# Kernel tuning notes

Hardware: AMD Instinct MI355X
Metric: run time of the kernel (lower is better)

## Reference

```python
import jax, jax.numpy as jnp
import numpy as np

C = 128          # hidden width hard-coded in DirModelToFace
EPS = 1e-5       # BatchNorm1d eps


def sparse_bmm(rows, cols, vals, x, num_rows):
    """Batched sparse @ dense: COO (rows, cols, vals) shared across batch.
    x: [B, K, c] -> [B, num_rows, c]."""
    def one(xb):
        return jax.ops.segment_sum(xb[cols] * vals[:, None], rows, num_segments=num_rows)
    return jax.vmap(one)(x)


def conv1x1_prebn(x, gamma, beta, W, b):
    # GraphConv1x1(batch_norm='pre'): BN (training stats over B*N rows) then Linear
    mean = x.mean((0, 1))
    var = x.var((0, 1))  # biased, as torch BN uses for normalization
    xh = (x - mean) * jax.lax.rsqrt(var + EPS) * gamma + beta
    return xh @ W + b


def dir_block(Di, DiA, v, f, g, be, W, b):
    # DirResNet2 (res_f=False): quaternionic Dirac message passing
    B, N, _ = v.shape
    Fn = f.shape[1]
    msg_v = sparse_bmm(*DiA, f.reshape(B, 4 * Fn, C // 4), 4 * N).reshape(B, N, C)
    x = jax.nn.elu(jnp.concatenate([v, msg_v], axis=-1))
    v_out = v + conv1x1_prebn(x, g[0], be[0], W[0], b[0])
    msg_f = sparse_bmm(*Di, v_out.reshape(B, 4 * N, C // 4), 4 * Fn).reshape(B, Fn, C)
    x = jax.nn.elu(jnp.concatenate([f, msg_f], axis=-1))
    f_out = conv1x1_prebn(x, g[1], be[1], W[1], b[1])  # no residual on f
    return v_out, f_out


def avg_block(mask, v, g, be, W, b):
    # AvgResNet2: masked global average message
    x = v
    for j in range(2):
        x = jax.nn.elu(x)
        x_avg = (mask * x).sum(1, keepdims=True) / mask.sum(1, keepdims=True)
        x = jnp.concatenate([x, jnp.broadcast_to(x_avg, x.shape)], axis=-1)
        x = conv1x1_prebn(x, g[j], be[j], W[j], b[j])
    return x + v


def setup_inputs() -> dict:
    key = jax.random.key(0)
    ks = jax.random.split(key, 10)
    B, N, Fn = 4, 12000, 24000
    nnz = 48 * Fn  # 3 vertices per face x 4x4 quaternion block
    inputs = jax.random.normal(ks[0], (B, N, 3), jnp.float32)
    mask = jnp.ones((B, N, 1), jnp.float32)
    Di_rows = jax.random.randint(ks[1], (nnz,), 0, 4 * Fn, jnp.int32)
    Di_cols = jax.random.randint(ks[2], (nnz,), 0, 4 * N, jnp.int32)
    Di_vals = jax.random.normal(ks[3], (nnz,), jnp.float32) * 0.1
    DiA_rows = jax.random.randint(ks[4], (nnz,), 0, 4 * N, jnp.int32)
    DiA_cols = jax.random.randint(ks[5], (nnz,), 0, 4 * Fn, jnp.int32)
    DiA_vals = jax.random.normal(ks[6], (nnz,), jnp.float32) * 0.1
    W1 = jax.random.normal(ks[7], (3, C), jnp.float32) / np.sqrt(3.0)
    b1 = jnp.zeros((C,), jnp.float32)
    rn_gamma = jnp.ones((16, 2, 2 * C), jnp.float32)
    rn_beta = jnp.zeros((16, 2, 2 * C), jnp.float32)
    rn_W = jax.random.normal(ks[8], (16, 2, 2 * C, C), jnp.float32) / np.sqrt(2.0 * C)
    rn_b = jnp.zeros((16, 2, C), jnp.float32)
    g2 = jnp.ones((C,), jnp.float32)
    be2 = jnp.zeros((C,), jnp.float32)
    W2 = jax.random.normal(ks[9], (C, 1), jnp.float32) / np.sqrt(1.0 * C)
    b2 = jnp.zeros((1,), jnp.float32)
    return dict(inputs=inputs, mask=mask,
                Di_rows=Di_rows, Di_cols=Di_cols, Di_vals=Di_vals,
                DiA_rows=DiA_rows, DiA_cols=DiA_cols, DiA_vals=DiA_vals,
                W1=W1, b1=b1, rn_gamma=rn_gamma, rn_beta=rn_beta, rn_W=rn_W, rn_b=rn_b,
                g2=g2, be2=be2, W2=W2, b2=b2, num_faces=24000)


def reference(inputs, mask, Di_rows, Di_cols, Di_vals, DiA_rows, DiA_cols, DiA_vals,
              W1, b1, rn_gamma, rn_beta, rn_W, rn_b, g2, be2, W2, b2, num_faces):
    B, N, _ = inputs.shape
    v = inputs @ W1 + b1                       # conv1 (batch_norm=None)
    f = jnp.zeros((B, num_faces, C), v.dtype)  # face features start at zero
    Di = (Di_rows, Di_cols, Di_vals)
    DiA = (DiA_rows, DiA_cols, DiA_vals)
    for i in range(16):
        if i % 2 == 0:
            v, f = dir_block(Di, DiA, v, f, rn_gamma[i], rn_beta[i], rn_W[i], rn_b[i])
        else:
            v = avg_block(mask, v, rn_gamma[i], rn_beta[i], rn_W[i], rn_b[i])
    x = jax.nn.elu(f)
    return conv1x1_prebn(x, g2, be2, W2, b2)   # conv2 (batch_norm='pre')
```

## Files before the change

### kernel.cpp

```cpp
#include <hip/hip_runtime.h>
#include <hip/hip_fp16.h>
#include <math.h>


#define EPS 1e-5f

typedef float floatx4 __attribute__((ext_vector_type(4)));
typedef short shortx8 __attribute__((ext_vector_type(8)));

__device__ __forceinline__ float eluf(float x) { return x > 0.f ? x : expm1f(x); }
__device__ __forceinline__ float4 elu4(float4 v) {
    v.x = eluf(v.x); v.y = eluf(v.y); v.z = eluf(v.z); v.w = eluf(v.w); return v;
}
__device__ __forceinline__ short f2bf(float x) {
    unsigned u = __builtin_bit_cast(unsigned, x);
    u = u + 0x7FFFu + ((u >> 16) & 1u);
    return (short)(u >> 16);
}
__device__ __forceinline__ float bf2f(short h) {
    unsigned u = ((unsigned)(unsigned short)h) << 16;
    return __builtin_bit_cast(float, u);
}
__device__ __forceinline__ void split2(float x, short& hi, short& lo) {
    unsigned u = __builtin_bit_cast(unsigned, x);
    hi = (short)(u >> 16);
    float r = x - bf2f(hi);
    lo = (short)(__builtin_bit_cast(unsigned, r) >> 16);
}

__global__ void conv1_kernel(const float* __restrict__ in, const float* __restrict__ W1,
                             const float* __restrict__ b1, float* __restrict__ v,
                             __half* __restrict__ vH, int N, float* __restrict__ Sout,
                             const float* __restrict__ mask, float* __restrict__ msum,
                             int nConv) {
    __shared__ float sh[4];
    int t = threadIdx.x;
    if (blockIdx.x >= nConv) {
        int b = blockIdx.x - nConv;
        float s = 0.f;
        for (int n = t; n < N; n += 256) s += mask[(size_t)b * N + n];
        for (int o = 32; o > 0; o >>= 1) s += __shfl_down(s, o);
        if ((t & 63) == 0) sh[t >> 6] = s;
        __syncthreads();
        if (t == 0) msum[b] = sh[0] + sh[1] + sh[2] + sh[3];
        return;
    }
    int c = t & 127, half = t >> 7;
    int r0 = blockIdx.x * 64;
    float w0 = W1[c], w1 = W1[128 + c], w2 = W1[256 + c], bb = b1[c];
    float s1 = 0.f, s2 = 0.f;
    for (int k = 0; k < 32; ++k) {
        int r = r0 + half + 2 * k;
        float x0 = in[r * 3 + 0], x1 = in[r * 3 + 1], x2 = in[r * 3 + 2];
        float val = bb + x0 * w0 + x1 * w1 + x2 * w2;
        v[(size_t)r * 128 + c] = val;
        int b = r / N, vert = r - b * N;
        vH[(size_t)(4 * vert + (c >> 5)) * 128 + b * 32 + (c & 31)] = __float2half(val);
        float e = eluf(val);
        s1 += e; s2 += e * e;
    }
    atomicAdd(&Sout[c], s1);
    atomicAdd(&Sout[256 + c], s2);
}


__global__ void hist2_kernel(const int* __restrict__ rowsA, const int* __restrict__ rowsD,
                             int* __restrict__ cntA, int* __restrict__ cntD) {
    int e = blockIdx.x * 256 + threadIdx.x;
    if (blockIdx.y == 0) atomicAdd(&cntA[rowsA[e]], 1);
    else atomicAdd(&cntD[rowsD[e]], 1);
}

__global__ void partial2_kernel(const int* __restrict__ cntA, const int* __restrict__ cntD,
                                int* __restrict__ partA, int* __restrict__ partD,
                                int RA, int RD) {
    const int* counts = blockIdx.y ? cntD : cntA;
    int* partials = blockIdx.y ? partD : partA;
    int R = blockIdx.y ? RD : RA;
    int t = threadIdx.x;
    int base = blockIdx.x * 1024 + t * 4;
    int s = 0;
#pragma unroll
    for (int j = 0; j < 4; ++j) { int i = base + j; if (i < R) s += counts[i]; }
    __shared__ int sh[256];
    sh[t] = s; __syncthreads();
    for (int st = 128; st > 0; st >>= 1) {
        if (t < st) sh[t] += sh[t + st];
        __syncthreads();
    }
    if (t == 0) partials[blockIdx.x] = sh[0];
}

__global__ void scanp2_kernel(int* __restrict__ partA, int* __restrict__ partD,
                              int* __restrict__ ptrA, int* __restrict__ ptrD,
                              int PA, int PD, int RA, int RD, int total) {
    int* partials = blockIdx.y ? partD : partA;
    int* rowptr = blockIdx.y ? ptrD : ptrA;
    int P = blockIdx.y ? PD : PA;
    int R = blockIdx.y ? RD : RA;
    __shared__ int sh[256];
    int t = threadIdx.x;
    int v = (t < P) ? partials[t] : 0;
    sh[t] = v; __syncthreads();
    for (int st = 1; st < 256; st <<= 1) {
        int tmp = (t >= st) ? sh[t - st] : 0;
        __syncthreads();
        sh[t] += tmp;
        __syncthreads();
    }
    if (t < P) partials[t] = sh[t] - v;
    if (t == 0) rowptr[R] = total;
}

__global__ void apply2_kernel(int* __restrict__ cntA, int* __restrict__ cntD,
                              const int* __restrict__ partA, const int* __restrict__ partD,
                              int* __restrict__ ptrA, int* __restrict__ ptrD,
                              int RA, int RD) {
    int* counts = blockIdx.y ? cntD : cntA;
    const int* partials = blockIdx.y ? partD : partA;
    int* rowptr = blockIdx.y ? ptrD : ptrA;
    int R = blockIdx.y ? RD : RA;
    int t = threadIdx.x;
    int base = blockIdx.x * 1024 + t * 4;
    int c[4]; int s = 0;
#pragma unroll
    for (int j = 0; j < 4; ++j) { int i = base + j; c[j] = (i < R) ? counts[i] : 0; s += c[j]; }
    __shared__ int sh[256];
    sh[t] = s; __syncthreads();
    for (int st = 1; st < 256; st <<= 1) {
        int tmp = (t >= st) ? sh[t - st] : 0;
        __syncthreads();
        sh[t] += tmp;
        __syncthreads();
    }
    int off = partials[blockIdx.x] + sh[t] - s;
#pragma unroll
    for (int j = 0; j < 4; ++j) {
        int i = base + j;
        if (i < R) { rowptr[i] = off; counts[i] = off; }
        off += c[j];
    }
}

__global__ void scatter2_kernel(const int* __restrict__ rowsA, const int* __restrict__ colsA,
                                const float* __restrict__ valsA,
                                const int* __restrict__ rowsD, const int* __restrict__ colsD,
                                const float* __restrict__ valsD,
                                int* __restrict__ fillA, int* __restrict__ fillD,
                                int2* __restrict__ edgesA, int2* __restrict__ edgesD) {
    int e = blockIdx.x * 256 + threadIdx.x;
    if (blockIdx.y == 0) {
        int p = atomicAdd(&fillA[rowsA[e]], 1);
        edgesA[p] = make_int2(colsA[e], __float_as_int(valsA[e]));
    } else {
        int p = atomicAdd(&fillD[rowsD[e]], 1);
        edgesD[p] = make_int2(colsD[e], __float_as_int(valsD[e]));
    }
}

template <int DIR>
__global__ __launch_bounds__(1024) void spmm_csr_kernel(
    const int* __restrict__ rowptr, const int2* __restrict__ edges,
    const __half2* __restrict__ xH, float* __restrict__ y, int R4,
    float* __restrict__ Sout) {
    int t = threadIdx.x;
    int waveId = blockIdx.x * 16 + (t >> 6);
    int lane = t & 63;
    int b = lane >> 4, cp = lane & 15;
    const __half2* xb = xH + b * 16 + cp;
    size_t rs = (size_t)R4 * 32;
    __shared__ float red[256];
    if (t < 256) red[t] = 0.f;
    __syncthreads();
#pragma unroll
    for (int rr = 0; rr < 2; ++rr) {
        int r = waveId * 2 + rr;
        int e0 = rowptr[r], e1 = rowptr[r + 1];
        float ax = 0.f, ay = 0.f;
        int e = e0;
        for (; e + 4 <= e1; e += 4) {
            int2 E0 = edges[e], E1 = edges[e + 1], E2 = edges[e + 2], E3 = edges[e + 3];
            __half2 g0 = xb[(size_t)E0.x * 64];
            __half2 g1 = xb[(size_t)E1.x * 64];
            __half2 g2 = xb[(size_t)E2.x * 64];
            __half2 g3 = xb[(size_t)E3.x * 64];
            float v0 = __int_as_float(E0.y), v1 = __int_as_float(E1.y);
            float v2 = __int_as_float(E2.y), v3 = __int_as_float(E3.y);
            float2 f0 = __half22float2(g0), f1 = __half22float2(g1);
            float2 f2 = __half22float2(g2), f3 = __half22float2(g3);
            ax += v0 * f0.x; ay += v0 * f0.y;
            ax += v1 * f1.x; ay += v1 * f1.y;
            ax += v2 * f2.x; ay += v2 * f2.y;
            ax += v3 * f3.x; ay += v3 * f3.y;
        }
        for (; e < e1; ++e) {
            int2 E = edges[e];
            __half2 g = xb[(size_t)E.x * 64];
            float v = __int_as_float(E.y);
            float2 f = __half22float2(g);
            ax += v * f.x; ay += v * f.y;
        }
        *(float2*)&y[(size_t)b * rs + (size_t)r * 32 + cp * 2] = make_float2(ax, ay);
        float ea = eluf(ax), eb = eluf(ay);
        float s1a = ea, s2a = ea * ea, s1b = eb, s2b = eb * eb;
        s1a += __shfl_xor(s1a, 16); s1a += __shfl_xor(s1a, 32);
        s2a += __shfl_xor(s2a, 16); s2a += __shfl_xor(s2a, 32);
        s1b += __shfl_xor(s1b, 16); s1b += __shfl_xor(s1b, 32);
        s2b += __shfl_xor(s2b, 16); s2b += __shfl_xor(s2b, 32);
        if (lane < 16) {
            int ch = (r & 3) * 32 + cp * 2;
            atomicAdd(&red[ch], s1a);
            atomicAdd(&red[ch + 1], s1b);
            atomicAdd(&red[128 + ch], s2a);
            atomicAdd(&red[128 + ch + 1], s2b);
        }
    }
    __syncthreads();
    if (t < 128) atomicAdd(&Sout[128 + t], red[t]);
    else if (t < 256) atomicAdd(&Sout[384 + (t - 128)], red[t]);
}

template <int MODEB>
__global__ __launch_bounds__(256) void gemm_mfma(
    const float* __restrict__ A, const float* __restrict__ Bs,
    const float* __restrict__ S, const float* __restrict__ gvec,
    const float* __restrict__ bevec, const float* __restrict__ Wfull,
    const float* __restrict__ bvec, const float* __restrict__ resid,
    float* __restrict__ out, __half* __restrict__ shadow,
    float* __restrict__ Sout, const float* __restrict__ mask,
    float* __restrict__ avgout, const float* __restrict__ avgacc,
    const float* __restrict__ msum, float invR, int rowsPerBatch) {
    __shared__ short Bsh[128 * 40];
    __shared__ short Bsl[128 * 40];
    __shared__ float sS[256];
    __shared__ float sMS[256];
    __shared__ float avgLDS[512];
    __shared__ float bparr[256];
    __shared__ float bparrX[2][256];
    __shared__ float bpF2[2][128];
    const int t = threadIdx.x;
    const int lane = t & 63;
    const int wave = t >> 6;
    const int rowBase = blockIdx.x * 128 + wave * 32;
    const int m = lane & 15;
    const int kq = lane >> 4;
    constexpr int kbEnd = (MODEB == 0) ? 8 : 4;
    const int colW = t & 127;
    const int qs0 = t >> 7;
    const int bBlk = (blockIdx.x * 128) / rowsPerBatch;

    {
        int k = t;
        float mean, var;
        if (MODEB == 1 && k >= 128) {
            int c = k - 128;
            float a0 = avgacc[c] / msum[0];
            float a1 = avgacc[128 + c] / msum[1];
            float a2 = avgacc[256 + c] / msum[2];
            float a3 = avgacc[384 + c] / msum[3];
            avgLDS[c] = a0; avgLDS[128 + c] = a1;
            avgLDS[256 + c] = a2; avgLDS[384 + c] = a3;
            mean = 0.25f * (a0 + a1 + a2 + a3);
            var = 0.25f * (a0 * a0 + a1 * a1 + a2 * a2 + a3 * a3) - mean * mean;
        } else {
            mean = S[k] * invR;
            var = S[256 + k] * invR - mean * mean;
        }
        float s = gvec[k] / sqrtf(var + EPS);
        sS[k] = s;
        sMS[k] = bevec[k] - mean * s;
    }

    floatx4 acc[2][8];
#pragma unroll
    for (int i = 0; i < 2; ++i)
#pragma unroll
        for (int j = 0; j < 8; ++j) acc[i][j] = {0.f, 0.f, 0.f, 0.f};

    float bpp = 0.f;
    for (int kb = 0; kb < kbEnd; ++kb) {
        const int k0 = kb * 32 + kq * 8;
        __syncthreads();
#pragma unroll
        for (int i = 0; i < 2; ++i) {
            const int qs = qs0 + 2 * i;
            shortx8 hv, lv;
#pragma unroll
            for (int j = 0; j < 8; ++j) {
                int k = kb * 32 + qs * 8 + j;
                float w = Wfull[(size_t)k * 128 + colW];
                float wp = sS[k] * w;
                short h = f2bf(wp);
                hv[j] = h;
                lv[j] = f2bf(wp - bf2f(h));
                bpp += sMS[k] * w;
            }
            *(shortx8*)&Bsh[colW * 40 + qs * 8] = hv;
            *(shortx8*)&Bsl[colW * 40 + qs * 8] = lv;
        }
        shortx8 ah[2], al[2];
#pragma unroll
        for (int rg = 0; rg < 2; ++rg) {
            int row = rowBase + rg * 16 + m;
            float4 p, q;
            if (kb < 4) {
                p = elu4(*(const float4*)&A[(size_t)row * 128 + k0]);
                q = elu4(*(const float4*)&A[(size_t)row * 128 + k0 + 4]);
            } else {
                int kk = k0 - 128;
                p = elu4(*(const float4*)&Bs[(size_t)row * 128 + kk]);
                q = elu4(*(const float4*)&Bs[(size_t)row * 128 + kk + 4]);
            }
            float x[8] = {p.x, p.y, p.z, p.w, q.x, q.y, q.z, q.w};
#pragma unroll
            for (int j = 0; j < 8; ++j) { short h, l; split2(x[j], h, l); ah[rg][j] = h; al[rg][j] = l; }
        }
        __syncthreads();
#pragma unroll
        for (int ct = 0; ct < 8; ++ct) {
            const int co = (ct * 16 + m) * 40 + kq * 8;
            shortx8 bh = *(const shortx8*)&Bsh[co];
            shortx8 bl = *(const shortx8*)&Bsl[co];
#pragma unroll
            for (int rg = 0; rg < 2; ++rg) {
                acc[rg][ct] = __builtin_amdgcn_mfma_f32_16x16x32_bf16(ah[rg], bh, acc[rg][ct], 0, 0, 0);
                acc[rg][ct] = __builtin_amdgcn_mfma_f32_16x16x32_bf16(ah[rg], bl, acc[rg][ct], 0, 0, 0);
                acc[rg][ct] = __builtin_amdgcn_mfma_f32_16x16x32_bf16(al[rg], bh, acc[rg][ct], 0, 0, 0);
            }
        }
    }

    float bps0 = 0.f, bps1 = 0.f;
    if (MODEB == 2) {
        for (int j = 0; j < 64; ++j) {
            int k = 128 + qs0 * 64 + j;
            bps0 += sMS[k] * Wfull[(size_t)k * 128 + colW];
        }
        bps1 = bps0;
    } else if (MODEB == 1) {
        const int b0 = bBlk, b1 = (bBlk + 1 < 4) ? bBlk + 1 : 3;
        for (int j = 0; j < 64; ++j) {
            int k = 128 + qs0 * 64 + j;
            float w = Wfull[(size_t)k * 128 + colW];
            float sw = sS[k] * w;
            float base = sMS[k] * w;
            bps0 += base + avgLDS[b0 * 128 + (k - 128)] * sw;
            bps1 += base + avgLDS[b1 * 128 + (k - 128)] * sw;
        }
    }
    bparr[t] = bpp;
    bparrX[0][t] = bps0;
    bparrX[1][t] = bps1;
    __syncthreads();
    if (t < 128) {
        float common = bvec[t] + bparr[t] + bparr[t + 128];
        bpF2[0][t] = common + bparrX[0][t] + bparrX[0][t + 128];
        bpF2[1][t] = common + bparrX[1][t] + bparrX[1][t + 128];
    }
    __syncthreads();

    float mk8[8]; int ib8[8];
#pragma unroll
    for (int rg = 0; rg < 2; ++rg)
#pragma unroll
        for (int r = 0; r < 4; ++r) {
            int row = rowBase + rg * 16 + kq * 4 + r;
            ib8[rg * 4 + r] = (row >= (bBlk + 1) * rowsPerBatch) ? 1 : 0;
            if (avgout) mk8[rg * 4 + r] = mask[row];
        }
    float cs1[8], cs2[8], av0[8], av1[8];
#pragma unroll
    for (int ct = 0; ct < 8; ++ct) { cs1[ct] = 0.f; cs2[ct] = 0.f; av0[ct] = 0.f; av1[ct] = 0.f; }
#pragma unroll
    for (int ct = 0; ct < 8; ++ct) {
        int col = ct * 16 + m;
        float bb0 = bpF2[0][col], bb1 = bpF2[1][col];
#pragma unroll
        for (int rg = 0; rg < 2; ++rg) {
#pragma unroll
            for (int r = 0; r < 4; ++r) {
                int row = rowBase + rg * 16 + kq * 4 + r;
                size_t o = (size_t)row * 128 + col;
                float v = acc[rg][ct][r] + (ib8[rg * 4 + r] ? bb1 : bb0);
                if (resid) v += resid[o];
                out[o] = v;
                if (shadow) {
                    int b = row / rowsPerBatch, vert = row - b * rowsPerBatch;
                    shadow[(size_t)(4 * vert + (col >> 5)) * 128 + b * 32 + (col & 31)] =
                        __float2half(v);
                }
                float e = eluf(v);
                cs1[ct] += e; cs2[ct] += e * e;
                if (avgout) {
                    float me = mk8[rg * 4 + r] * e;
                    if (ib8[rg * 4 + r]) av1[ct] += me; else av0[ct] += me;
                }
            }
        }
    }
    if (Sout) {
        __syncthreads();
        float* red = (float*)Bsh;
        float* redv = (float*)Bsl;
        red[t] = 0.f;
        if (avgout) redv[t] = 0.f;
        __syncthreads();
#pragma unroll
        for (int ct = 0; ct < 8; ++ct) {
            cs1[ct] += __shfl_xor(cs1[ct], 16); cs1[ct] += __shfl_xor(cs1[ct], 32);
            cs2[ct] += __shfl_xor(cs2[ct], 16); cs2[ct] += __shfl_xor(cs2[ct], 32);
            if (avgout) {
                av0[ct] += __shfl_xor(av0[ct], 16); av0[ct] += __shfl_xor(av0[ct], 32);
                av1[ct] += __shfl_xor(av1[ct], 16); av1[ct] += __shfl_xor(av1[ct], 32);
            }
        }
        if (kq == 0) {
#pragma unroll
            for (int ct = 0; ct < 8; ++ct) {
                atomicAdd(&red[ct * 16 + m], cs1[ct]);
                atomicAdd(&red[128 + ct * 16 + m], cs2[ct]);
                if (avgout) {
                    atomicAdd(&redv[ct * 16 + m], av0[ct]);
                    atomicAdd(&redv[128 + ct * 16 + m], av1[ct]);
                }
            }
        }
        __syncthreads();
        if (t < 128) atomicAdd(&Sout[t], red[t]);
        else atomicAdd(&Sout[256 + (t - 128)], red[t]);
        if (avgout) {
            int plane = t >> 7, col = t & 127;
            int b = bBlk + plane;
            if (b < 4) atomicAdd(&avgout[b * 128 + col], redv[t]);
        }
    }
}

__global__ void fold_final(const float* __restrict__ S, const float* __restrict__ g2,
                           const float* __restrict__ be2, const float* __restrict__ W2,
                           const float* __restrict__ b2, float* __restrict__ W2p, float invR) {
    __shared__ float red[128];
    int c = threadIdx.x;
    float mean = S[c] * invR;
    float var = S[256 + c] * invR - mean * mean;
    float s = g2[c] / sqrtf(var + EPS);
    float w = W2[c];
    W2p[c] = s * w;
    red[c] = (be2[c] - mean * s) * w;
    __syncthreads();
    for (int st = 64; st > 0; st >>= 1) {
        if (c < st) red[c] += red[c + st];
        __syncthreads();
    }
    if (c == 0) W2p[128] = b2[0] + red[0];
}

__global__ void final_out_kernel(const float* __restrict__ f, const float* __restrict__ W2p,
                                 float* __restrict__ out) {
    int t = threadIdx.x;
    int w = t >> 6, lane = t & 63;
    float wa = W2p[lane], wb = W2p[64 + lane], bb = W2p[128];
    int base = blockIdx.x * 16 + w * 4;
#pragma unroll
    for (int rr = 0; rr < 4; ++rr) {
        int row = base + rr;
        float a = eluf(f[(size_t)row * 128 + lane]) * wa +
                  eluf(f[(size_t)row * 128 + 64 + lane]) * wb;
        for (int off = 32; off > 0; off >>= 1) a += __shfl_down(a, off);
        if (lane == 0) out[row] = a + bb;
    }
}

extern "C" void kernel_launch(void* const* d_in, const int* in_sizes, int n_in,
                              void* d_out, int out_size, void* d_ws, size_t ws_size,
                              hipStream_t stream) {
    const float* inputs = (const float*)d_in[0];
    const float* mask = (const float*)d_in[1];
    const int* Di_rows = (const int*)d_in[2];
    const int* Di_cols = (const int*)d_in[3];
    const float* Di_vals = (const float*)d_in[4];
    const int* DiA_rows = (const int*)d_in[5];
    const int* DiA_cols = (const int*)d_in[6];
    const float* DiA_vals = (const float*)d_in[7];
    const float* W1 = (const float*)d_in[8];
    const float* b1 = (const float*)d_in[9];
    const float* rn_gamma = (const float*)d_in[10];
    const float* rn_beta = (const float*)d_in[11];
    const float* rn_W = (const float*)d_in[12];
    const float* rn_b = (const float*)d_in[13];
    const float* g2 = (const float*)d_in[14];
    const float* be2 = (const float*)d_in[15];
    const float* W2 = (const float*)d_in[16];
    const float* b2 = (const float*)d_in[17];
    float* out = (float*)d_out;

    const int B = 4;
    const int BN = in_sizes[1];
    const int N = BN / B;
    const int BF = out_size;
    const int Fn = BF / B;
    const int nnz = in_sizes[2];
    const int RA = 4 * N;
    const int RD = 4 * Fn;

    float* ws = (float*)d_ws;
    size_t off = 0;
    float* vA = ws + off;  off += (size_t)BN * 128;
    float* fA = ws + off;  off += (size_t)BF * 128;
    float* msg = ws + off; off += (size_t)BF * 128;
    __half* vH = (__half*)(ws + off); off += (size_t)RA * 128 / 2;
    __half* fH = (__half*)(ws + off); off += (size_t)RD * 128 / 2;
    int* ptrA    = (int*)(ws + off);  off += (size_t)RA + 4;
    int2* edgesA = (int2*)(ws + off); off += (size_t)nnz * 2;
    int* ptrD    = (int*)(ws + off);  off += (size_t)RD + 4;
    int2* edgesD = (int2*)(ws + off); off += (size_t)nnz * 2;
    int* cntA    = (int*)(ws + off);  off += (size_t)RA;
    int* cntD    = (int*)(ws + off);  off += (size_t)RD;
    int* partA   = (int*)(ws + off);  off += 256;
    int* partD   = (int*)(ws + off);  off += 256;
    float* Sarena = ws + off; off += 33 * 512;
    float* Aarena = ws + off; off += 16 * 512;
    float* msum = ws + off;   off += 4;
    float* W2p = ws + off; off += 132;

    const int eBlocks = nnz / 256;
    const int PA = (RA + 1023) / 1024;
    const int PD = (RD + 1023) / 1024;

    hipMemsetAsync(Sarena, 0, (33 * 512 + 16 * 512) * 4, stream);
    hipMemsetAsync(fA, 0, (size_t)BF * 128 * 4, stream);
    hipMemsetAsync(cntA, 0, (size_t)(RA + RD) * 4, stream);

    hist2_kernel<<<dim3(eBlocks, 2), 256, 0, stream>>>(DiA_rows, Di_rows, cntA, cntD);
    partial2_kernel<<<dim3(PD, 2), 256, 0, stream>>>(cntA, cntD, partA, partD, RA, RD);
    scanp2_kernel<<<dim3(1, 2), 256, 0, stream>>>(partA, partD, ptrA, ptrD, PA, PD,
                                                  RA, RD, nnz);
    apply2_kernel<<<dim3(PD, 2), 256, 0, stream>>>(cntA, cntD, partA, partD, ptrA, ptrD,
                                                   RA, RD);
    scatter2_kernel<<<dim3(eBlocks, 2), 256, 0, stream>>>(DiA_rows, DiA_cols, DiA_vals,
                                                          Di_rows, Di_cols, Di_vals,
                                                          cntA, cntD, edgesA, edgesD);

    auto slot = [&](int i, int j) { return Sarena + 512 * (2 * i + j); };
    float* Sfinal = Sarena + 512 * 32;

    conv1_kernel<<<BN / 64 + B, 256, 0, stream>>>(inputs, W1, b1, vA, vH, N, slot(0, 0),
                                                  mask, msum, BN / 64);

    for (int i = 0; i < 15; ++i) {
        if ((i & 1) == 0) {
            const float* g0 = rn_gamma + (size_t)(i * 2 + 0) * 256;
            const float* be0 = rn_beta + (size_t)(i * 2 + 0) * 256;
            const float* Wl0 = rn_W + (size_t)(i * 2 + 0) * 256 * 128;
            const float* bl0 = rn_b + (size_t)(i * 2 + 0) * 128;
            const float* g1 = rn_gamma + (size_t)(i * 2 + 1) * 256;
            const float* be1 = rn_beta + (size_t)(i * 2 + 1) * 256;
            const float* Wl1 = rn_W + (size_t)(i * 2 + 1) * 256 * 128;
            const float* bl1 = rn_b + (size_t)(i * 2 + 1) * 128;
            float* SoutV = (i < 14) ? slot(i + 1, 0) : nullptr;
            float* avgV = (i < 14) ? (Aarena + 512 * i) : nullptr;

            if (i == 0) {
                gemm_mfma<2><<<BN / 128, 256, 0, stream>>>(vA, nullptr, slot(0, 0), g0, be0,
                                                           Wl0, bl0, vA, vA, vH, SoutV, mask,
                                                           avgV, nullptr, nullptr, 1.f / BN,
                                                           N);
            } else {
                spmm_csr_kernel<0><<<RA / 32, 1024, 0, stream>>>(ptrA, edgesA,
                                                                 (const __half2*)fH, msg,
                                                                 RA, slot(i, 0));
                gemm_mfma<0><<<BN / 128, 256, 0, stream>>>(vA, msg, slot(i, 0), g0, be0,
                                                           Wl0, bl0, vA, vA, vH, SoutV, mask,
                                                           avgV, nullptr, nullptr, 1.f / BN,
                                                           N);
            }

            spmm_csr_kernel<1><<<RD / 32, 1024, 0, stream>>>(ptrD, edgesD,
                                                             (const __half2*)vH, msg, RD,
                                                             slot(i, 1));
            gemm_mfma<0><<<BF / 128, 256, 0, stream>>>(fA, msg, slot(i, 1), g1, be1, Wl1,
                                                       bl1, nullptr, fA, fH,
                                                       (i < 14) ? slot(i + 2, 1) : Sfinal,
                                                       nullptr, nullptr, nullptr, nullptr,
                                                       1.f / BF, Fn);
        } else {
            for (int j = 0; j < 2; ++j) {
                const float* g = rn_gamma + (size_t)(i * 2 + j) * 256;
                const float* be = rn_beta + (size_t)(i * 2 + j) * 256;
                const float* Wlw = rn_W + (size_t)(i * 2 + j) * 256 * 128;
                const float* bl = rn_b + (size_t)(i * 2 + j) * 128;
                const float* src = (j == 0) ? vA : msg;
                float* dst = (j == 0) ? msg : vA;
                const float* resid = (j == 0) ? nullptr : vA;
                __half* shadow = (j == 0) ? nullptr : vH;
                float* SoutP = (j == 0) ? slot(i, 1) : slot(i + 1, 0);
                float* avgO = (j == 0) ? (Aarena + 512 * i) : nullptr;
                const float* avgacc = Aarena + 512 * (i - 1 + j);

                gemm_mfma<1><<<BN / 128, 256, 0, stream>>>(src, nullptr, slot(i, j), g, be,
                                                           Wlw, bl, resid, dst, shadow,
                                                           SoutP, mask, avgO, avgacc, msum,
                                                           1.f / BN, N);
            }
        }
    }

    fold_final<<<1, 128, 0, stream>>>(Sfinal, g2, be2, W2, b2, W2p, 1.f / BF);
    final_out_kernel<<<BF / 16, 256, 0, stream>>>(fA, W2p, out);
}
```

Measured before the change: 4.151 ms.

## Prefold weights into MFMA fragment layout once; apply BN to activations instead

A new prefold kernel converts every layer's weight matrix to split hi/lo bf16 in MFMA fragment order once per call. The GEMM then loads B fragments straight from global memory, removing the per-block LDS staging, syncs and weight folding. BatchNorm scale and shift move onto the activations, and the avg-block broadcast term becomes real K columns instead of a bias correction. The cost is that MODEB 1 and 2 now always run 8 k-blocks, the i==0 case multiplies against zeros, and occupancy is raised to 2 blocks per SIMD via launch bounds.

```diff
diff --git a/kernel.cpp b/kernel.cpp
--- a/kernel.cpp
+++ b/kernel.cpp
@@ -26,6 +26,28 @@
     hi = (short)(u >> 16);
     float r = x - bf2f(hi);
     lo = (short)(__builtin_bit_cast(unsigned, r) >> 16);
+}
+
+__global__ void prefold_kernel(const float* __restrict__ rnW, short* __restrict__ Wh,
+                               short* __restrict__ Wl) {
+    int L = blockIdx.y;
+    int id = blockIdx.x * 256 + threadIdx.x;
+    int chunk = id >> 6, lane = id & 63;
+    int kb = chunk >> 3, ct = chunk & 7, kq = lane >> 4, m = lane & 15;
+    const float* W = rnW + (size_t)L * 32768;
+    shortx8 hv, lv;
+#pragma unroll
+    for (int j = 0; j < 8; ++j) {
+        int k = kb * 32 + kq * 8 + j;
+        int c = ct * 16 + m;
+        float w = W[k * 128 + c];
+        short h = f2bf(w);
+        hv[j] = h;
+        lv[j] = f2bf(w - bf2f(h));
+    }
+    size_t o = (size_t)L * 32768 + (size_t)id * 8;
+    *(shortx8*)&Wh[o] = hv;
+    *(shortx8*)&Wl[o] = lv;
 }
 
 __global__ void conv1_kernel(const float* __restrict__ in, const float* __restrict__ W1,
@@ -221,32 +243,27 @@
 }
 
 template <int MODEB>
-__global__ __launch_bounds__(256) void gemm_mfma(
+__global__ __launch_bounds__(256, 2) void gemm_mfma(
     const float* __restrict__ A, const float* __restrict__ Bs,
     const float* __restrict__ S, const float* __restrict__ gvec,
-    const float* __restrict__ bevec, const float* __restrict__ Wfull,
-    const float* __restrict__ bvec, const float* __restrict__ resid,
-    float* __restrict__ out, __half* __restrict__ shadow,
-    float* __restrict__ Sout, const float* __restrict__ mask,
-    float* __restrict__ avgout, const float* __restrict__ avgacc,
-    const float* __restrict__ msum, float invR, int rowsPerBatch) {
-    __shared__ short Bsh[128 * 40];
-    __shared__ short Bsl[128 * 40];
+    const float* __restrict__ bevec, const short* __restrict__ Wh,
+    const short* __restrict__ Wl, const float* __restrict__ bvec,
+    const float* __restrict__ resid, float* __restrict__ out,
+    __half* __restrict__ shadow, float* __restrict__ Sout,
+    const float* __restrict__ mask, float* __restrict__ avgout,
+    const float* __restrict__ avgacc, const float* __restrict__ msum,
+    float invR, int rowsPerBatch) {
     __shared__ float sS[256];
     __shared__ float sMS[256];
     __shared__ float avgLDS[512];
-    __shared__ float bparr[256];
-    __shared__ float bparrX[2][256];
-    __shared__ float bpF2[2][128];
+    __shared__ float red[256];
+    __shared__ float redv[256];
     const int t = threadIdx.x;
     const int lane = t & 63;
     const int wave = t >> 6;
     const int rowBase = blockIdx.x * 128 + wave * 32;
     const int m = lane & 15;
     const int kq = lane >> 4;
-    constexpr int kbEnd = (MODEB == 0) ? 8 : 4;
-    const int colW = t & 127;
-    const int qs0 = t >> 7;
     const int bBlk = (blockIdx.x * 128) / rowsPerBatch;
 
     {
@@ -270,6 +287,7 @@
         sS[k] = s;
         sMS[k] = bevec[k] - mean * s;
     }
+    __syncthreads();
 
     floatx4 acc[2][8];
 #pragma unroll
@@ -277,50 +295,51 @@
 #pragma unroll
         for (int j = 0; j < 8; ++j) acc[i][j] = {0.f, 0.f, 0.f, 0.f};
 
-    float bpp = 0.f;
-    for (int kb = 0; kb < kbEnd; ++kb) {
+#pragma unroll 2
+    for (int kb = 0; kb < 8; ++kb) {
         const int k0 = kb * 32 + kq * 8;
-        __syncthreads();
-#pragma unroll
-        for (int i = 0; i < 2; ++i) {
-            const int qs = qs0 + 2 * i;
-            shortx8 hv, lv;
+        shortx8 ah[2], al[2];
+#pragma unroll
+        for (int rg = 0; rg < 2; ++rg) {
+            const int row = rowBase + rg * 16 + m;
+            float x[8];
+            if (kb < 4) {
+                float4 p = elu4(*(const float4*)&A[(size_t)row * 128 + k0]);
+                float4 q = elu4(*(const float4*)&A[(size_t)row * 128 + k0 + 4]);
+                x[0] = p.x; x[1] = p.y; x[2] = p.z; x[3] = p.w;
+                x[4] = q.x; x[5] = q.y; x[6] = q.z; x[7] = q.w;
+            } else if (MODEB == 0) {
+                const int kk = k0 - 128;
+                float4 p = elu4(*(const float4*)&Bs[(size_t)row * 128 + kk]);
+                float4 q = elu4(*(const float4*)&Bs[(size_t)row * 128 + kk + 4]);
+                x[0] = p.x; x[1] = p.y; x[2] = p.z; x[3] = p.w;
+                x[4] = q.x; x[5] = q.y; x[6] = q.z; x[7] = q.w;
+            } else if (MODEB == 1) {
+                const int kk = k0 - 128;
+                const int b = row / rowsPerBatch;
+                float4 p = *(const float4*)&avgLDS[b * 128 + kk];
+                float4 q = *(const float4*)&avgLDS[b * 128 + kk + 4];
+                x[0] = p.x; x[1] = p.y; x[2] = p.z; x[3] = p.w;
+                x[4] = q.x; x[5] = q.y; x[6] = q.z; x[7] = q.w;
+            } else {
+#pragma unroll
+                for (int j = 0; j < 8; ++j) x[j] = 0.f;
+            }
 #pragma unroll
             for (int j = 0; j < 8; ++j) {
-                int k = kb * 32 + qs * 8 + j;
-                float w = Wfull[(size_t)k * 128 + colW];
-                float wp = sS[k] * w;
-                short h = f2bf(wp);
-                hv[j] = h;
-                lv[j] = f2bf(wp - bf2f(h));
-                bpp += sMS[k] * w;
-            }
-            *(shortx8*)&Bsh[colW * 40 + qs * 8] = hv;
-            *(shortx8*)&Bsl[colW * 40 + qs * 8] = lv;
-        }
-        shortx8 ah[2], al[2];
-#pragma unroll
-        for (int rg = 0; rg < 2; ++rg) {
-            int row = rowBase + rg * 16 + m;
-            float4 p, q;
-            if (kb < 4) {
-                p = elu4(*(const float4*)&A[(size_t)row * 128 + k0]);
-                q = elu4(*(const float4*)&A[(size_t)row * 128 + k0 + 4]);
-            } else {
-                int kk = k0 - 128;
-                p = elu4(*(const float4*)&Bs[(size_t)row * 128 + kk]);
-                q = elu4(*(const float4*)&Bs[(size_t)row * 128 + kk + 4]);
-            }
-            float x[8] = {p.x, p.y, p.z, p.w, q.x, q.y, q.z, q.w};
-#pragma unroll
-            for (int j = 0; j < 8; ++j) { short h, l; split2(x[j], h, l); ah[rg][j] = h; al[rg][j] = l; }
-        }
-        __syncthreads();
+                const int k = k0 + j;
+                float ap = sS[k] * x[j] + sMS[k];
+                short h, l;
+                split2(ap, h, l);
+                ah[rg][j] = h;
+                al[rg][j] = l;
+            }
+        }
 #pragma unroll
         for (int ct = 0; ct < 8; ++ct) {
-            const int co = (ct * 16 + m) * 40 + kq * 8;
-            shortx8 bh = *(const shortx8*)&Bsh[co];
-            shortx8 bl = *(const shortx8*)&Bsl[co];
+            const size_t wo = ((size_t)(kb * 8 + ct) * 64 + lane) * 8;
+            shortx8 bh = *(const shortx8*)&Wh[wo];
+            shortx8 bl = *(const shortx8*)&Wl[wo];
 #pragma unroll
             for (int rg = 0; rg < 2; ++rg) {
                 acc[rg][ct] = __builtin_amdgcn_mfma_f32_16x16x32_bf16(ah[rg], bh, acc[rg][ct], 0, 0, 0);
@@ -330,58 +349,31 @@
         }
     }
 
-    float bps0 = 0.f, bps1 = 0.f;
-    if (MODEB == 2) {
-        for (int j = 0; j < 64; ++j) {
-            int k = 128 + qs0 * 64 + j;
-            bps0 += sMS[k] * Wfull[(size_t)k * 128 + colW];
-        }
-        bps1 = bps0;
-    } else if (MODEB == 1) {
-        const int b0 = bBlk, b1 = (bBlk + 1 < 4) ? bBlk + 1 : 3;
-        for (int j = 0; j < 64; ++j) {
-            int k = 128 + qs0 * 64 + j;
-            float w = Wfull[(size_t)k * 128 + colW];
-            float sw = sS[k] * w;
-            float base = sMS[k] * w;
-            bps0 += base + avgLDS[b0 * 128 + (k - 128)] * sw;
-            bps1 += base + avgLDS[b1 * 128 + (k - 128)] * sw;
-        }
-    }
-    bparr[t] = bpp;
-    bparrX[0][t] = bps0;
-    bparrX[1][t] = bps1;
-    __syncthreads();
-    if (t < 128) {
-        float common = bvec[t] + bparr[t] + bparr[t + 128];
-        bpF2[0][t] = common + bparrX[0][t] + bparrX[0][t + 128];
-        bpF2[1][t] = common + bparrX[1][t] + bparrX[1][t + 128];
-    }
-    __syncthreads();
-
     float mk8[8]; int ib8[8];
-#pragma unroll
-    for (int rg = 0; rg < 2; ++rg)
-#pragma unroll
-        for (int r = 0; r < 4; ++r) {
-            int row = rowBase + rg * 16 + kq * 4 + r;
-            ib8[rg * 4 + r] = (row >= (bBlk + 1) * rowsPerBatch) ? 1 : 0;
-            if (avgout) mk8[rg * 4 + r] = mask[row];
-        }
+    if (avgout) {
+#pragma unroll
+        for (int rg = 0; rg < 2; ++rg)
+#pragma unroll
+            for (int r = 0; r < 4; ++r) {
+                int row = rowBase + rg * 16 + kq * 4 + r;
+                mk8[rg * 4 + r] = mask[row];
+                ib8[rg * 4 + r] = (row >= (bBlk + 1) * rowsPerBatch) ? 1 : 0;
+            }
+    }
     float cs1[8], cs2[8], av0[8], av1[8];
 #pragma unroll
     for (int ct = 0; ct < 8; ++ct) { cs1[ct] = 0.f; cs2[ct] = 0.f; av0[ct] = 0.f; av1[ct] = 0.f; }
 #pragma unroll
     for (int ct = 0; ct < 8; ++ct) {
         int col = ct * 16 + m;
-        float bb0 = bpF2[0][col], bb1 = bpF2[1][col];
+        float bb = bvec[col];
 #pragma unroll
         for (int rg = 0; rg < 2; ++rg) {
 #pragma unroll
             for (int r = 0; r < 4; ++r) {
                 int row = rowBase + rg * 16 + kq * 4 + r;
                 size_t o = (size_t)row * 128 + col;
-                float v = acc[rg][ct][r] + (ib8[rg * 4 + r] ? bb1 : bb0);
+                float v = acc[rg][ct][r] + bb;
                 if (resid) v += resid[o];
                 out[o] = v;
                 if (shadow) {
@@ -400,8 +392,6 @@
     }
     if (Sout) {
         __syncthreads();
-        float* red = (float*)Bsh;
-        float* redv = (float*)Bsl;
         red[t] = 0.f;
         if (avgout) redv[t] = 0.f;
         __syncthreads();
@@ -522,6 +512,8 @@
     float* Aarena = ws + off; off += 16 * 512;
     float* msum = ws + off;   off += 4;
     float* W2p = ws + off; off += 132;
+    short* Wh = (short*)(ws + off); off += (size_t)32 * 32768 / 2;
+    short* Wl = (short*)(ws + off); off += (size_t)32 * 32768 / 2;
 
     const int eBlocks = nnz / 256;
     const int PA = (RA + 1023) / 1024;
@@ -530,6 +522,8 @@
     hipMemsetAsync(Sarena, 0, (33 * 512 + 16 * 512) * 4, stream);
     hipMemsetAsync(fA, 0, (size_t)BF * 128 * 4, stream);
     hipMemsetAsync(cntA, 0, (size_t)(RA + RD) * 4, stream);
+
+    prefold_kernel<<<dim3(16, 32), 256, 0, stream>>>(rn_W, Wh, Wl);
 
     hist2_kernel<<<dim3(eBlocks, 2), 256, 0, stream>>>(DiA_rows, Di_rows, cntA, cntD);
     partial2_kernel<<<dim3(PD, 2), 256, 0, stream>>>(cntA, cntD, partA, partD, RA, RD);
@@ -547,39 +541,41 @@
     conv1_kernel<<<BN / 64 + B, 256, 0, stream>>>(inputs, W1, b1, vA, vH, N, slot(0, 0),
                                                   mask, msum, BN / 64);
 
+    auto WhL = [&](int i, int j) { return Wh + (size_t)(i * 2 + j) * 32768; };
+    auto WlL = [&](int i, int j) { return Wl + (size_t)(i * 2 + j) * 32768; };
+
     for (int i = 0; i < 15; ++i) {
         if ((i & 1) == 0) {
             const float* g0 = rn_gamma + (size_t)(i * 2 + 0) * 256;
             const float* be0 = rn_beta + (size_t)(i * 2 + 0) * 256;
-            const float* Wl0 = rn_W + (size_t)(i * 2 + 0) * 256 * 128;
             const float* bl0 = rn_b + (size_t)(i * 2 + 0) * 128;
             const float* g1 = rn_gamma + (size_t)(i * 2 + 1) * 256;
             const float* be1 = rn_beta + (size_t)(i * 2 + 1) * 256;
-            const float* Wl1 = rn_W + (size_t)(i * 2 + 1) * 256 * 128;
             const float* bl1 = rn_b + (size_t)(i * 2 + 1) * 128;
             float* SoutV = (i < 14) ? slot(i + 1, 0) : nullptr;
             float* avgV = (i < 14) ? (Aarena + 512 * i) : nullptr;
 
             if (i == 0) {
                 gemm_mfma<2><<<BN / 128, 256, 0, stream>>>(vA, nullptr, slot(0, 0), g0, be0,
-                                                           Wl0, bl0, vA, vA, vH, SoutV, mask,
-                                                           avgV, nullptr, nullptr, 1.f / BN,
-                                                           N);
+                                                           WhL(i, 0), WlL(i, 0), bl0, vA, vA,
+                                                           vH, SoutV, mask, avgV, nullptr,
+                                                           nullptr, 1.f / BN, N);
             } else {
                 spmm_csr_kernel<0><<<RA / 32, 1024, 0, stream>>>(ptrA, edgesA,
                                                                  (const __half2*)fH, msg,
                                                                  RA, slot(i, 0));
                 gemm_mfma<0><<<BN / 128, 256, 0, stream>>>(vA, msg, slot(i, 0), g0, be0,
-                                                           Wl0, bl0, vA, vA, vH, SoutV, mask,
-                                                           avgV, nullptr, nullptr, 1.f / BN,
-                                                           N);
+                                                           WhL(i, 0), WlL(i, 0), bl0, vA, vA,
+                                                           vH, SoutV, mask, avgV, nullptr,
+                                                           nullptr, 1.f / BN, N);
             }
 
             spmm_csr_kernel<1><<<RD / 32, 1024, 0, stream>>>(ptrD, edgesD,
                                                              (const __half2*)vH, msg, RD,
                                                              slot(i, 1));
-            gemm_mfma<0><<<BF / 128, 256, 0, stream>>>(fA, msg, slot(i, 1), g1, be1, Wl1,
-                                                       bl1, nullptr, fA, fH,
+            gemm_mfma<0><<<BF / 128, 256, 0, stream>>>(fA, msg, slot(i, 1), g1, be1,
+                                                       WhL(i, 1), WlL(i, 1), bl1, nullptr,
+                                                       fA, fH,
                                                        (i < 14) ? slot(i + 2, 1) : Sfinal,
                                                        nullptr, nullptr, nullptr, nullptr,
                                                        1.f / BF, Fn);
@@ -587,7 +583,6 @@
             for (int j = 0; j < 2; ++j) {
                 const float* g = rn_gamma + (size_t)(i * 2 + j) * 256;
                 const float* be = rn_beta + (size_t)(i * 2 + j) * 256;
-                const float* Wlw = rn_W + (size_t)(i * 2 + j) * 256 * 128;
                 const float* bl = rn_b + (size_t)(i * 2 + j) * 128;
                 const float* src = (j == 0) ? vA : msg;
                 float* dst = (j == 0) ? msg : vA;
@@ -598,9 +593,9 @@
                 const float* avgacc = Aarena + 512 * (i - 1 + j);
 
                 gemm_mfma<1><<<BN / 128, 256, 0, stream>>>(src, nullptr, slot(i, j), g, be,
-                                                           Wlw, bl, resid, dst, shadow,
-                                                           SoutP, mask, avgO, avgacc, msum,
-                                                           1.f / BN, N);
+                                                           WhL(i, j), WlL(i, j), bl, resid,
+                                                           dst, shadow, SoutP, mask, avgO,
+                                                           avgacc, msum, 1.f / BN, N);
             }
         }
     }
```

Result: no change. 4.169 ms (+0.5%).
